# Optimization experiments

Measured on AMD Instinct MI355X. Metric: run time of the kernel, lower is better.

## Reference

```python
import jax, jax.numpy as jnp
import numpy as np

N_NODES = 20000
N_EDGES = 320000
N_RELS = 200
DESC_LEN = 16
DIM_G = 64
DIM_WORD = 300
DIM_HIDDEN = 256
H_DIR = DIM_HIDDEN // 2  # per-direction GRU hidden
N_CLASS = 2000
V_WORD = 30000
V_DESC = 30000
B, T = 4, 32


def setup_inputs() -> dict:
    key = jax.random.key(0)
    ks = jax.random.split(key, 24)
    inp = {}
    # index tensors (pad token is 0; generate tokens in [1, V) so all positions valid)
    inp['questions'] = jax.random.randint(ks[0], (B, T), 1, V_WORD)
    inp['node_descs'] = jax.random.randint(ks[1], (N_NODES, DESC_LEN), 1, V_DESC)
    inp['edge_src'] = jax.random.randint(ks[2], (N_EDGES,), 0, N_NODES)
    inp['edge_dst'] = jax.random.randint(ks[3], (N_EDGES,), 0, N_NODES)
    inp['edge_type'] = jax.random.randint(ks[4], (N_EDGES,), 0, N_RELS)
    # embeddings (normal with std 1/sqrt(dim) as in original init)
    inp['emb_word'] = jax.random.normal(ks[5], (V_WORD, DIM_WORD)) / np.sqrt(DIM_WORD)
    inp['emb_desc'] = jax.random.normal(ks[6], (V_DESC, DIM_G)) / np.sqrt(DIM_G)
    # BiGRU params (gates order r,z,n; concatenated along last dim)
    s = 0.1
    inp['Wx_f'] = jax.random.normal(ks[7], (DIM_WORD, 3 * H_DIR)) * s
    inp['Wh_f'] = jax.random.normal(ks[8], (H_DIR, 3 * H_DIR)) * s
    inp['bx_f'] = jnp.zeros((3 * H_DIR,))
    inp['bh_f'] = jnp.zeros((3 * H_DIR,))
    inp['Wx_b'] = jax.random.normal(ks[9], (DIM_WORD, 3 * H_DIR)) * s
    inp['Wh_b'] = jax.random.normal(ks[10], (H_DIR, 3 * H_DIR)) * s
    inp['bx_b'] = jnp.zeros((3 * H_DIR,))
    inp['bh_b'] = jnp.zeros((3 * H_DIR,))
    # lin_h_to_g (kaiming-ish scale)
    inp['W_hg'] = jax.random.normal(ks[11], (DIM_HIDDEN, DIM_G)) * np.sqrt(2.0 / DIM_HIDDEN)
    inp['b_hg'] = jnp.zeros((DIM_G,))
    # RGCN basis decomposition
    inp['bases'] = jax.random.normal(ks[12], (1, DIM_G, DIM_G)) * np.sqrt(1.0 / DIM_G)
    inp['w_comp'] = jax.random.normal(ks[13], (N_RELS, 1))
    inp['rgcn_bias'] = jnp.zeros((DIM_G,))
    # classifier
    inp['W1'] = jax.random.normal(ks[14], (DIM_G + DIM_HIDDEN, 1024)) * np.sqrt(2.0 / (DIM_G + DIM_HIDDEN))
    inp['b1'] = jnp.zeros((1024,))
    inp['W2'] = jax.random.normal(ks[15], (1024, N_CLASS)) * np.sqrt(2.0 / 1024)
    inp['b2'] = jnp.zeros((N_CLASS,))
    return inp


def _gru_last_hidden(x, mask, Wx, Wh, bx, bh):
    """Run a GRU over time; hidden only updates where mask is True.
    x: [B,T,D], mask: [B,T]. Returns final hidden [B,H]."""
    bsz = x.shape[0]
    h0 = jnp.zeros((bsz, Wh.shape[0]), x.dtype)
    gx_all = x @ Wx + bx  # [B,T,3H] precompute input gates

    def step(h, inputs):
        gx, mt = inputs  # [B,3H], [B]
        gh = h @ Wh + bh
        xr, xz, xn = jnp.split(gx, 3, axis=-1)
        hr, hz, hn = jnp.split(gh, 3, axis=-1)
        r = jax.nn.sigmoid(xr + hr)
        z = jax.nn.sigmoid(xz + hz)
        n = jnp.tanh(xn + r * hn)
        h_new = (1.0 - z) * n + z * h
        h = jnp.where(mt[:, None], h_new, h)
        return h, None

    hT, _ = jax.lax.scan(step, h0, (gx_all.transpose(1, 0, 2), mask.T))
    return hT


def _rel_graph_conv(h, edge_src, edge_dst, edge_type, bases, w_comp, bias):
    """Basis-decomposed RGCN layer (DGL RelGraphConv, norm=None, no self-loop).
    h: [B,N,G]. W_r = sum_k w_comp[r,k] * bases[k]."""
    n = h.shape[1]
    # project through each basis first: [B,N,K,O]
    hb = jnp.einsum('bng,kgo->bnko', h, bases)
    # per-edge message: gather src, combine with relation coefficients -> [B,E,O]
    msg = jnp.einsum('beko,ek->beo', hb[:, edge_src], w_comp[edge_type])
    # scatter-add to destination nodes
    agg = jax.vmap(lambda m: jax.ops.segment_sum(m, edge_dst, num_segments=n))(msg)
    return jax.nn.relu(agg + bias)


def reference(questions, node_descs, edge_src, edge_dst, edge_type,
              emb_word, emb_desc,
              Wx_f, Wh_f, bx_f, bh_f, Wx_b, Wh_b, bx_b, bh_b,
              W_hg, b_hg, bases, w_comp, rgcn_bias,
              W1, b1, W2, b2):
    # ---- question encoding (BiGRU over non-pad tokens; pad id = 0) ----
    mask = questions != 0  # [B,T]
    x = emb_word[questions]  # [B,T,Dw] (dropout is identity at eval)
    hf = _gru_last_hidden(x, mask, Wx_f, Wh_f, bx_f, bh_f)
    hb = _gru_last_hidden(x[:, ::-1], mask[:, ::-1], Wx_b, Wh_b, bx_b, bh_b)
    q_emb = jnp.concatenate([hf, hb], axis=-1)  # [B, dim_hidden]

    # ---- attention-weighted node features from descriptions ----
    desc_emb = emb_desc[node_descs]          # [N,L,G]
    q_g = q_emb @ W_hg + b_hg                # [B,G]
    attn1 = jax.nn.softmax(jnp.einsum('nlg,bg->bnl', desc_emb, q_g), axis=-1)
    node_feat = jnp.einsum('bnl,nlg->bng', attn1, desc_emb)  # [B,N,G]

    # ---- one RGCN hidden layer over the KB graph ----
    node_feat = _rel_graph_conv(node_feat, edge_src, edge_dst, edge_type,
                                bases, w_comp, rgcn_bias)

    # ---- attention pooling over nodes ----
    attn2 = jax.nn.softmax(jnp.einsum('bng,bg->bn', node_feat, q_g), axis=1)
    node_agg = jnp.einsum('bn,bng->bg', attn2, node_feat)    # [B,G]

    # ---- classifier ----
    feat = jnp.concatenate([node_agg, q_emb], axis=-1)       # [B, G+H]
    logits = jax.nn.relu(feat @ W1 + b1) @ W2 + b2           # [B, n_class]
    return logits
```

## Files before the change

### kernel.cpp

```cpp
#include <hip/hip_runtime.h>
#include <hip/hip_bf16.h>
#include <math.h>

typedef __hip_bfloat16 bf16;

#define NNODES 20000
#define NEDGES 320000
#define DLEN   16
#define G      64
#define DW     300
#define DH     256
#define HD     128
#define G3     384
#define NCLS   2000
#define NB     4
#define TT     32
#define A2BLK  1024
#define A2MID  64

#define NBLK_CVT  384
#define NBLK_GX2  1536
#define NBLK_HIST ((NEDGES + 255) / 256)
#define NBLK_SCAT ((NEDGES + 255) / 256)

__device__ __forceinline__ float ld(const float* p, size_t i) { return p[i]; }
__device__ __forceinline__ float ld(const bf16* p, size_t i) { return __bfloat162float(p[i]); }
__device__ __forceinline__ void st(float* p, size_t i, float v) { p[i] = v; }
__device__ __forceinline__ void st(bf16* p, size_t i, float v) { p[i] = __float2bfloat16(v); }
__device__ __forceinline__ float relu(float x) { return (x < 0.f) ? 0.f : x; }

struct __align__(8) bf4 { bf16 x, y, z, w; };

#define OFF_FLAG  ((size_t)0)
#define OFF_GX    (OFF_FLAG + 4)
#define OFF_WHF   (OFF_GX   + 2*NB*TT*G3)
#define OFF_QEMB  (OFF_WHF  + 2*HD*G3)
#define OFF_QG    (OFF_QEMB + NB*DH)
#define OFF_NF    (OFF_QG   + NB*G)
#define OFF_HB    (OFF_NF   + (size_t)NB*NNODES*G)
#define OFF_PART  (OFF_HB   + (size_t)NB*NNODES*G)
#define OFF_PART2 (OFF_PART + (size_t)A2BLK*NB*66)
#define OFF_DEG   (OFF_PART2+ (size_t)A2MID*NB*66)
#define OFF_OFFS  (OFF_DEG  + NNODES)
#define OFF_CUR   (OFF_OFFS + NNODES + 8)
#define OFF_SSRC  (OFF_CUR  + NNODES)
#define OFF_SCO   (OFF_SSRC + NEDGES)
#define OFF_HID   (OFF_SCO  + NEDGES)

__global__ void k_init(const unsigned* probe, int* flag, int* deg) {
    int i = blockIdx.x * 256 + threadIdx.x;
    if (i < NNODES) deg[i] = 0;
    if (blockIdx.x == 0 && threadIdx.x < 64) {
        int cnt = 0;
        for (int k = threadIdx.x; k < 4096; k += 64) {
            unsigned lo = probe[k] & 0xFFFFu;
            unsigned e = (lo >> 7) & 0xFFu;
            cnt += (e >= 0x66u && e <= 0x7Eu) ? 1 : 0;
        }
#pragma unroll
        for (int off = 1; off < 64; off <<= 1) cnt += __shfl_xor(cnt, off, 64);
        if (threadIdx.x == 0) *flag = (2 * cnt > 4096) ? 1 : 0;
    }
}

template <typename T>
__device__ void cvt_body(int id, const void* Whf_, const void* Whb_, float* whf) {
    if (id >= 2 * HD * G3) return;
    int d = id / (HD * G3), r = id % (HD * G3);
    const T* W = (const T*)(d ? Whb_ : Whf_);
    whf[id] = ld(W, (size_t)r);
}

template <typename T>
__device__ void gx2_body(int bx2, const int* questions, const void* emb_word_,
                         const void* Wxf_, const void* bxf_,
                         const void* Wxb_, const void* bxb_, float* gx,
                         float* xs, float* psum) {
    int tid = threadIdx.x;
    int jt = bx2 % 6;
    int rid = bx2 / 6;
    int step = rid & 31;
    int b = (rid >> 5) & 3;
    int d = rid >> 7;
    int t = d ? (TT - 1 - step) : step;
    int tok = questions[b * TT + t];
    const T* row = (const T*)emb_word_ + (size_t)tok * DW;
    for (int k = tid; k < DW; k += 256) xs[k] = ld(row, (size_t)k);
    __syncthreads();
    int lane = tid & 63, phase = tid >> 6;
    int j = jt * 64 + lane;
    const T* Wx = (const T*)(d ? Wxb_ : Wxf_);
    float acc = 0.f;
    int k0 = phase * 75;
#pragma unroll 15
    for (int kk = 0; kk < 75; kk++) {
        int k = k0 + kk;
        acc += xs[k] * ld(Wx, (size_t)k * G3 + j);
    }
    psum[tid] = acc;
    __syncthreads();
    if (phase == 0) {
        const T* bx = (const T*)(d ? bxb_ : bxf_);
        float tot = ld(bx, (size_t)j)
                  + psum[lane] + psum[64 + lane] + psum[128 + lane] + psum[192 + lane];
        gx[(size_t)rid * G3 + j] = tot;
    }
}

__global__ void k_prep(const int* flag, const void* Whf, const void* Whb, float* whf,
                       const int* questions, const void* emb_word,
                       const void* Wxf, const void* bxf,
                       const void* Wxb, const void* bxb, float* gx,
                       const int* edge_dst, int* deg) {
    __shared__ float xs[DW];
    __shared__ float psum[256];
    int bx = blockIdx.x;
    int tid = threadIdx.x;
    if (bx < NBLK_CVT) {
        int id = bx * 256 + tid;
        if (*flag) cvt_body<bf16>(id, Whf, Whb, whf);
        else       cvt_body<float>(id, Whf, Whb, whf);
    } else if (bx < NBLK_CVT + NBLK_GX2) {
        int bx2 = bx - NBLK_CVT;
        if (*flag) gx2_body<bf16>(bx2, questions, emb_word, Wxf, bxf, Wxb, bxb, gx, xs, psum);
        else       gx2_body<float>(bx2, questions, emb_word, Wxf, bxf, Wxb, bxb, gx, xs, psum);
    } else {
        int e = (bx - NBLK_CVT - NBLK_GX2) * 256 + tid;
        if (e < NEDGES) atomicAdd(&deg[edge_dst[e]], 1);
    }
}

template <typename T>
__device__ void gru_body(const int* questions, const float* gx, const float* whf,
                         const void* bhf_, const void* bhb_, float* qemb,
                         float* hsm, float* ghs) {
    int tid = threadIdx.x;
    int d = blockIdx.x >> 2, b = blockIdx.x & 3;
    int half = tid / G3, j = tid - half * G3;
    const float* wh = whf + (size_t)d * HD * G3 + (size_t)half * 64 * G3 + j;
    float w[64];
#pragma unroll
    for (int m = 0; m < 64; m++) w[m] = wh[(size_t)m * G3];
    const T* bh = (const T*)(d ? bhb_ : bhf_);
    float bhj = (half == 0) ? ld(bh, (size_t)j) : 0.f;
    if (tid < HD) hsm[tid] = 0.f;
    const float* gxb = gx + ((size_t)(d * NB + b)) * TT * G3;
    __syncthreads();
    const float4* h4 = (const float4*)(hsm + half * 64);
    for (int step = 0; step < TT; step++) {
        float acc = bhj;
#pragma unroll
        for (int m4 = 0; m4 < 16; m4++) {
            float4 hp = h4[m4];
            acc = fmaf(hp.x, w[4 * m4 + 0], acc);
            acc = fmaf(hp.y, w[4 * m4 + 1], acc);
            acc = fmaf(hp.z, w[4 * m4 + 2], acc);
            acc = fmaf(hp.w, w[4 * m4 + 3], acc);
        }
        ghs[half * G3 + j] = acc;
        __syncthreads();
        if (tid < HD) {
            const float* gxp = gxb + step * G3;
            int t = d ? (TT - 1 - step) : step;
            bool msk = questions[b * TT + t] != 0;
            float gr = ghs[tid] + ghs[G3 + tid];
            float gz = ghs[HD + tid] + ghs[G3 + HD + tid];
            float gn = ghs[2 * HD + tid] + ghs[G3 + 2 * HD + tid];
            float r = 1.f / (1.f + expf(-(gxp[tid] + gr)));
            float z = 1.f / (1.f + expf(-(gxp[HD + tid] + gz)));
            float n = tanhf(gxp[2 * HD + tid] + r * gn);
            float hn = (1.f - z) * n + z * hsm[tid];
            if (msk) hsm[tid] = hn;
        }
        __syncthreads();
    }
    if (tid < HD) qemb[b * DH + d * HD + tid] = hsm[tid];
}

__device__ void scan_body(const int* deg, int* offs, int* cur, int* wtot) {
    int t = threadIdx.x;
    int lane = t & 63, wave = t >> 6;
    int c[27];
    int base = t * 27;
    int run = 0;
#pragma unroll
    for (int i = 0; i < 27; i++) {
        int v = (base + i < NNODES) ? deg[base + i] : 0;
        c[i] = run;
        run += v;
    }
    int myrun = run, inc = run;
#pragma unroll
    for (int off = 1; off < 64; off <<= 1) {
        int u = __shfl_up(inc, off, 64);
        if (lane >= off) inc += u;
    }
    if (lane == 63) wtot[wave] = inc;
    __syncthreads();
    if (t == 0) {
        int s = 0;
#pragma unroll
        for (int i = 0; i < 12; i++) { int v = wtot[i]; wtot[i] = s; s += v; }
        offs[NNODES] = s;
    }
    __syncthreads();
    int ebase = wtot[wave] + inc - myrun;
#pragma unroll
    for (int i = 0; i < 27; i++) {
        if (base + i < NNODES) {
            offs[base + i] = ebase + c[i];
            cur[base + i] = ebase + c[i];
        }
    }
}

__global__ __launch_bounds__(2 * G3) void k_gru(const int* flag, const int* questions,
                                                const float* gx, const float* whf,
                                                const void* bhf, const void* bhb, float* qemb,
                                                const int* deg, int* offs, int* cur) {
    __shared__ __align__(16) float hsm[HD];
    __shared__ float ghs[2 * G3];
    __shared__ int wtot[12];
    if (blockIdx.x < 8) {
        if (*flag) gru_body<bf16>(questions, gx, whf, bhf, bhb, qemb, hsm, ghs);
        else       gru_body<float>(questions, gx, whf, bhf, bhb, qemb, hsm, ghs);
    } else {
        scan_body(deg, offs, cur, wtot);
    }
}

template <typename T>
__device__ void qg_body(const float* qemb, const void* W_hg_, const void* b_hg_, float* qg) {
    int tid = threadIdx.x;
    int b = tid >> 6, g = tid & 63;
    const T* W = (const T*)W_hg_;
    float acc = ld((const T*)b_hg_, (size_t)g);
#pragma unroll 4
    for (int i = 0; i < DH; i++) acc += qemb[b * DH + i] * ld(W, (size_t)i * G + g);
    qg[b * G + g] = acc;
}
__global__ void k_qg(const int* flag, const float* qemb, const void* W_hg,
                     const void* b_hg, float* qg) {
    if (*flag) qg_body<bf16>(qemb, W_hg, b_hg, qg);
    else       qg_body<float>(qemb, W_hg, b_hg, qg);
}

template <typename T>
__device__ void scatter_body(int e, const int* src, const int* dst, const int* typ,
                             const void* w_comp_, int* cur, int* ssrc, float* sco) {
    if (e < NEDGES) {
        int dd = dst[e];
        int pos = atomicAdd(&cur[dd], 1);
        ssrc[pos] = src[e];
        sco[pos] = ld((const T*)w_comp_, (size_t)typ[e]);
    }
}

template <typename T>
__device__ void attn1_body(int nb4, const int* node_descs, const void* emb_desc_,
                           const float* qg, bf16* nf16,
                           float* dsm, float* attn_s, float* qgs) {
    int tid = threadIdx.x;
    if (tid < NB * G) qgs[tid] = qg[tid];
    __syncthreads();
    const T* emb_desc = (const T*)emb_desc_;
    int w = tid >> 6, lane = tid & 63;
    int n = nb4 * 4 + w;
    float dreg[DLEN];
    const int* nd = node_descs + n * DLEN;
    float* dw = dsm + (size_t)w * DLEN * 68;
#pragma unroll
    for (int l = 0; l < DLEN; l++) {
        int idx = nd[l];
        float v = ld(emb_desc, (size_t)idx * G + lane);
        dreg[l] = v;
        dw[l * 68 + lane] = v;
    }
    int lb = lane >> 4, ll = lane & 15;
    float acc = 0.f;
#pragma unroll
    for (int i = 0; i < 16; i++) {
        float4 a = *(const float4*)&dw[ll * 68 + 4 * i];
        float4 q = *(const float4*)&qgs[lb * G + 4 * i];
        acc = fmaf(a.x, q.x, acc);
        acc = fmaf(a.y, q.y, acc);
        acc = fmaf(a.z, q.z, acc);
        acc = fmaf(a.w, q.w, acc);
    }
    float mx = acc;
#pragma unroll
    for (int off = 1; off < 16; off <<= 1) mx = fmaxf(mx, __shfl_xor(mx, off, 64));
    float e = expf(acc - mx);
    float s = e;
#pragma unroll
    for (int off = 1; off < 16; off <<= 1) s += __shfl_xor(s, off, 64);
    attn_s[w * 64 + lane] = e / s;
#pragma unroll
    for (int b = 0; b < NB; b++) {
        float a = 0.f;
#pragma unroll
        for (int l = 0; l < DLEN; l++) a += attn_s[w * 64 + b * 16 + l] * dreg[l];
        nf16[((size_t)b * NNODES + n) * G + lane] = __float2bfloat16(a);
    }
}

__global__ __launch_bounds__(256) void k_sc_attn1(const int* flag,
                                                  const int* src, const int* dst, const int* typ,
                                                  const void* w_comp, int* cur,
                                                  int* ssrc, float* sco,
                                                  const int* node_descs, const void* emb_desc,
                                                  const float* qg, bf16* nf16) {
    __shared__ __align__(16) float dsm[4 * DLEN * 68];
    __shared__ float attn_s[4 * 64];
    __shared__ __align__(16) float qgs[NB * G];
    int bx = blockIdx.x;
    if (bx < NBLK_SCAT) {
        int e = bx * 256 + threadIdx.x;
        if (*flag) scatter_body<bf16>(e, src, dst, typ, w_comp, cur, ssrc, sco);
        else       scatter_body<float>(e, src, dst, typ, w_comp, cur, ssrc, sco);
    } else {
        int nb4 = bx - NBLK_SCAT;
        if (*flag) attn1_body<bf16>(nb4, node_descs, emb_desc, qg, nf16, dsm, attn_s, qgs);
        else       attn1_body<float>(nb4, node_descs, emb_desc, qg, nf16, dsm, attn_s, qgs);
    }
}

template <typename T>
__device__ void hbg_body(const bf16* nf16, const void* bases_, bf16* hb16,
                         float* as, float* bs) {
    int tid = threadIdx.x;
    const T* bases = (const T*)bases_;
    for (int i = tid; i < G * G; i += 256) bs[(i >> 6) * 68 + (i & 63)] = ld(bases, (size_t)i);
    size_t r0 = (size_t)blockIdx.x * 64;
    const bf4* gA = (const bf4*)(nf16 + r0 * G);
#pragma unroll
    for (int i = 0; i < 4; i++) {
        int c = tid + i * 256;
        int row = c >> 4, col4 = c & 15;
        bf4 v = gA[c];
        float4 f;
        f.x = __bfloat162float(v.x);
        f.y = __bfloat162float(v.y);
        f.z = __bfloat162float(v.z);
        f.w = __bfloat162float(v.w);
        *(float4*)&as[row * 68 + col4 * 4] = f;
    }
    __syncthreads();
    int tx = tid & 15, ty = tid >> 4;
    float acc[4][4];
#pragma unroll
    for (int i = 0; i < 4; i++)
#pragma unroll
        for (int j = 0; j < 4; j++) acc[i][j] = 0.f;
#pragma unroll 4
    for (int g4 = 0; g4 < 16; g4++) {
        float4 b0 = *(const float4*)&bs[(4 * g4 + 0) * 68 + tx * 4];
        float4 b1 = *(const float4*)&bs[(4 * g4 + 1) * 68 + tx * 4];
        float4 b2 = *(const float4*)&bs[(4 * g4 + 2) * 68 + tx * 4];
        float4 b3 = *(const float4*)&bs[(4 * g4 + 3) * 68 + tx * 4];
#pragma unroll
        for (int i = 0; i < 4; i++) {
            float4 a = *(const float4*)&as[(ty * 4 + i) * 68 + g4 * 4];
            acc[i][0] = fmaf(a.x, b0.x, acc[i][0]);
            acc[i][0] = fmaf(a.y, b1.x, acc[i][0]);
            acc[i][0] = fmaf(a.z, b2.x, acc[i][0]);
            acc[i][0] = fmaf(a.w, b3.x, acc[i][0]);
            acc[i][1] = fmaf(a.x, b0.y, acc[i][1]);
            acc[i][1] = fmaf(a.y, b1.y, acc[i][1]);
            acc[i][1] = fmaf(a.z, b2.y, acc[i][1]);
            acc[i][1] = fmaf(a.w, b3.y, acc[i][1]);
            acc[i][2] = fmaf(a.x, b0.z, acc[i][2]);
            acc[i][2] = fmaf(a.y, b1.z, acc[i][2]);
            acc[i][2] = fmaf(a.z, b2.z, acc[i][2]);
            acc[i][2] = fmaf(a.w, b3.z, acc[i][2]);
            acc[i][3] = fmaf(a.x, b0.w, acc[i][3]);
            acc[i][3] = fmaf(a.y, b1.w, acc[i][3]);
            acc[i][3] = fmaf(a.z, b2.w, acc[i][3]);
            acc[i][3] = fmaf(a.w, b3.w, acc[i][3]);
        }
    }
#pragma unroll
    for (int i = 0; i < 4; i++) {
        size_t r = r0 + ty * 4 + i;
        int b = (int)(r / NNODES);
        int n = (int)(r - (size_t)b * NNODES);
        bf4 o;
        o.x = __float2bfloat16(acc[i][0]);
        o.y = __float2bfloat16(acc[i][1]);
        o.z = __float2bfloat16(acc[i][2]);
        o.w = __float2bfloat16(acc[i][3]);
        *(bf4*)&hb16[((size_t)n * NB + b) * G + tx * 4] = o;
    }
}
__global__ __launch_bounds__(256) void k_hbg(const int* flag, const bf16* nf16,
                                             const void* bases, bf16* hb16) {
    __shared__ __align__(16) float as[64 * 68];
    __shared__ __align__(16) float bs[64 * 68];
    if (*flag) hbg_body<bf16>(nf16, bases, hb16, as, bs);
    else       hbg_body<float>(nf16, bases, hb16, as, bs);
}

template <typename T>
__device__ void agg_body(const bf16* hb16, const int* offs, const int* ssrc,
                         const float* sco, const void* bias_, bf16* out_nf16) {
    int tid = threadIdx.x;
    int b = tid >> 6, g = tid & 63;
    int dn = blockIdx.x;
    int s0 = offs[dn], s1 = offs[dn + 1];
    int boff = b * G + g;
    float acc = 0.f;
    int p = s0;
    for (; p + 15 < s1; p += 16) {
        int ix[16]; float co[16]; float x[16];
#pragma unroll
        for (int k = 0; k < 16; k++) { ix[k] = ssrc[p + k]; co[k] = sco[p + k]; }
#pragma unroll
        for (int k = 0; k < 16; k++) x[k] = __bfloat162float(hb16[(size_t)ix[k] * (NB * G) + boff]);
#pragma unroll
        for (int k = 0; k < 16; k++) acc += co[k] * x[k];
    }
    for (; p + 7 < s1; p += 8) {
        int ix[8]; float co[8]; float x[8];
#pragma unroll
        for (int k = 0; k < 8; k++) { ix[k] = ssrc[p + k]; co[k] = sco[p + k]; }
#pragma unroll
        for (int k = 0; k < 8; k++) x[k] = __bfloat162float(hb16[(size_t)ix[k] * (NB * G) + boff]);
#pragma unroll
        for (int k = 0; k < 8; k++) acc += co[k] * x[k];
    }
    for (; p + 3 < s1; p += 4) {
        int ix[4]; float co[4]; float x[4];
#pragma unroll
        for (int k = 0; k < 4; k++) { ix[k] = ssrc[p + k]; co[k] = sco[p + k]; }
#pragma unroll
        for (int k = 0; k < 4; k++) x[k] = __bfloat162float(hb16[(size_t)ix[k] * (NB * G) + boff]);
#pragma unroll
        for (int k = 0; k < 4; k++) acc += co[k] * x[k];
    }
    for (; p < s1; p++)
        acc += sco[p] * __bfloat162float(hb16[(size_t)ssrc[p] * (NB * G) + boff]);
    out_nf16[((size_t)b * NNODES + dn) * G + g] =
        __float2bfloat16(relu(acc + ld((const T*)bias_, (size_t)g)));
}
__global__ __launch_bounds__(256) void k_agg(const int* flag, const bf16* hb16, const int* offs,
                                             const int* ssrc, const float* sco,
                                             const void* bias, bf16* out_nf16) {
    if (*flag) agg_body<bf16>(hb16, offs, ssrc, sco, bias, out_nf16);
    else       agg_body<float>(hb16, offs, ssrc, sco, bias, out_nf16);
}

__device__ __forceinline__ void a2_update(float& M, float& L, float& A, float p, float v) {
    if (p > M) {
        float s = expf(M - p);
        A *= s; L *= s; M = p;
    }
    float e = expf(p - M);
    L += e;
    A = fmaf(e, v, A);
}

__global__ __launch_bounds__(256) void k_attn2(const bf16* rg, const float* qg, float* part) {
    int tid = threadIdx.x;
    int b = tid >> 6, lane = tid & 63;
    float q = qg[b * G + lane];
    int chunk = (NNODES + A2BLK - 1) / A2BLK;
    int n0 = blockIdx.x * chunk;
    int n1 = min(n0 + chunk, NNODES);
    const bf16* base = rg + (size_t)b * NNODES * G + lane;
    float M = -3.4e38f, L = 0.f, A = 0.f;
    int n = n0;
    for (; n + 3 < n1; n += 4) {
        float v0 = __bfloat162float(base[(size_t)(n + 0) * G]);
        float v1 = __bfloat162float(base[(size_t)(n + 1) * G]);
        float v2 = __bfloat162float(base[(size_t)(n + 2) * G]);
        float v3 = __bfloat162float(base[(size_t)(n + 3) * G]);
        float p0 = v0 * q, p1 = v1 * q, p2 = v2 * q, p3 = v3 * q;
#pragma unroll
        for (int off = 32; off >= 1; off >>= 1) {
            p0 += __shfl_xor(p0, off, 64);
            p1 += __shfl_xor(p1, off, 64);
            p2 += __shfl_xor(p2, off, 64);
            p3 += __shfl_xor(p3, off, 64);
        }
        a2_update(M, L, A, p0, v0);
        a2_update(M, L, A, p1, v1);
        a2_update(M, L, A, p2, v2);
        a2_update(M, L, A, p3, v3);
    }
    for (; n < n1; n++) {
        float v = __bfloat162float(base[(size_t)n * G]);
        float p = v * q;
#pragma unroll
        for (int off = 32; off >= 1; off >>= 1) p += __shfl_xor(p, off, 64);
        a2_update(M, L, A, p, v);
    }
    float* pp = part + ((size_t)blockIdx.x * NB + b) * 66;
    if (lane == 0) { pp[0] = M; pp[1] = L; }
    pp[2 + lane] = A;
}

__global__ void k_attn2m(const float* part, float* part2) {
    int tid = threadIdx.x;
    int b = tid >> 6, lane = tid & 63;
    int grp = blockIdx.x;
    float M = -3.4e38f, L = 0.f, A = 0.f;
    for (int i = 0; i < A2BLK / A2MID; i++) {
        const float* pp = part + ((size_t)(grp * (A2BLK / A2MID) + i) * NB + b) * 66;
        float m = pp[0], l = pp[1], a = pp[2 + lane];
        float mn = fmaxf(M, m);
        float e1 = expf(M - mn), e2 = expf(m - mn);
        A = A * e1 + a * e2;
        L = L * e1 + l * e2;
        M = mn;
    }
    float* pq = part2 + ((size_t)grp * NB + b) * 66;
    if (lane == 0) { pq[0] = M; pq[1] = L; }
    pq[2 + lane] = A;
}

template <typename T>
__device__ void fc1_body(const float* part2, const float* qemb,
                         const void* W1_, const void* b1_, float* hid,
                         float* feat, float* psum) {
    int tid = threadIdx.x;
    int b = blockIdx.x >> 4, tile = blockIdx.x & 15;
    if (tid < 64) {
        float M = -3.4e38f, L = 0.f, A = 0.f;
        for (int p = 0; p < A2MID; p++) {
            const float* pp = part2 + ((size_t)p * NB + b) * 66;
            float m = pp[0], l = pp[1], a = pp[2 + tid];
            float mn = fmaxf(M, m);
            float e1 = expf(M - mn), e2 = expf(m - mn);
            A = A * e1 + a * e2;
            L = L * e1 + l * e2;
            M = mn;
        }
        feat[tid] = A / L;
        feat[tid + 256] = qemb[b * DH + tid + 192];
    } else {
        feat[tid] = qemb[b * DH + tid - G];
    }
    __syncthreads();
    int lane = tid & 63, phase = tid >> 6;
    int u = tile * 64 + lane;
    const T* W1 = (const T*)W1_;
    float acc = 0.f;
#pragma unroll 8
    for (int kk = 0; kk < 80; kk++) {
        int k = phase * 80 + kk;
        acc += feat[k] * ld(W1, (size_t)k * 1024 + u);
    }
    psum[tid] = acc;
    __syncthreads();
    if (phase == 0) {
        float tot = psum[lane] + psum[64 + lane] + psum[128 + lane] + psum[192 + lane]
                  + ld((const T*)b1_, (size_t)u);
        hid[b * 1024 + u] = relu(tot);
    }
}
__global__ __launch_bounds__(256) void k_fc1(const int* flag, const float* part2,
                                             const float* qemb, const void* W1, const void* b1,
                                             float* hid) {
    __shared__ float feat[320];
    __shared__ float psum[256];
    if (*flag) fc1_body<bf16>(part2, qemb, W1, b1, hid, feat, psum);
    else       fc1_body<float>(part2, qemb, W1, b1, hid, feat, psum);
}

template <typename T>
__device__ void fc2_body(const float* hid, const void* W2_, const void* b2_, void* out_,
                         float* hs, float* psum) {
    int tid = threadIdx.x;
    int tile = blockIdx.x;
#pragma unroll
    for (int i = 0; i < 16; i++) hs[tid + 256 * i] = hid[tid + 256 * i];
    __syncthreads();
    int lane = tid & 63, phase = tid >> 6;
    int c = tile * 64 + lane;
    bool ok = (c < NCLS);
    const T* W2 = (const T*)W2_;
    float a0 = 0.f, a1 = 0.f, a2 = 0.f, a3 = 0.f;
    if (ok) {
#pragma unroll 8
        for (int uu = 0; uu < 256; uu++) {
            int u = phase * 256 + uu;
            float w = ld(W2, (size_t)u * NCLS + c);
            a0 += hs[u] * w;
            a1 += hs[1024 + u] * w;
            a2 += hs[2048 + u] * w;
            a3 += hs[3072 + u] * w;
        }
    }
    psum[tid] = a0;
    psum[256 + tid] = a1;
    psum[512 + tid] = a2;
    psum[768 + tid] = a3;
    __syncthreads();
    if (phase == 0 && ok) {
        float bb = ld((const T*)b2_, (size_t)c);
#pragma unroll
        for (int b = 0; b < NB; b++) {
            float* ps = psum + b * 256;
            float tot = ps[lane] + ps[64 + lane] + ps[128 + lane] + ps[192 + lane] + bb;
            st((T*)out_, (size_t)b * NCLS + c, tot);
        }
    }
}
__global__ __launch_bounds__(256) void k_fc2(const int* flag, const float* hid,
                                             const void* W2, const void* b2v, void* out) {
    __shared__ float hs[4096];
    __shared__ float psum[1024];
    if (*flag) fc2_body<bf16>(hid, W2, b2v, out, hs, psum);
    else       fc2_body<float>(hid, W2, b2v, out, hs, psum);
}

extern "C" void kernel_launch(void* const* d_in, const int* in_sizes, int n_in,
                              void* d_out, int out_size, void* d_ws, size_t ws_size,
                              hipStream_t stream) {
    const int* questions  = (const int*)d_in[0];
    const int* node_descs = (const int*)d_in[1];
    const int* edge_src   = (const int*)d_in[2];
    const int* edge_dst   = (const int*)d_in[3];
    const int* edge_type  = (const int*)d_in[4];
    const void* emb_word  = d_in[5];
    const void* emb_desc  = d_in[6];
    const void* Wx_f = d_in[7];
    const void* Wh_f = d_in[8];
    const void* bx_f = d_in[9];
    const void* bh_f = d_in[10];
    const void* Wx_b = d_in[11];
    const void* Wh_b = d_in[12];
    const void* bx_b = d_in[13];
    const void* bh_b = d_in[14];
    const void* W_hg = d_in[15];
    const void* b_hg = d_in[16];
    const void* bases = d_in[17];
    const void* w_comp = d_in[18];
    const void* rgcn_bias = d_in[19];
    const void* W1 = d_in[20];
    const void* b1 = d_in[21];
    const void* W2 = d_in[22];
    const void* b2 = d_in[23];

    float* ws = (float*)d_ws;
    int*      flag  = (int*)(ws + OFF_FLAG);
    float*    gx    = ws + OFF_GX;
    float*    whf   = ws + OFF_WHF;
    float*    qemb  = ws + OFF_QEMB;
    float*    qg    = ws + OFF_QG;
    bf16*     nf16  = (bf16*)(ws + OFF_NF);
    bf16*     hb16  = (bf16*)(ws + OFF_HB);
    float*    part  = ws + OFF_PART;
    float*    part2 = ws + OFF_PART2;
    int*      deg   = (int*)(ws + OFF_DEG);
    int*      offs  = (int*)(ws + OFF_OFFS);
    int*      cur   = (int*)(ws + OFF_CUR);
    int*      ssrc  = (int*)(ws + OFF_SSRC);
    float*    sco   = ws + OFF_SCO;
    float*    hid   = ws + OFF_HID;

    hipLaunchKernelGGL(k_init, dim3(80), dim3(256), 0, stream,
                       (const unsigned*)emb_word, flag, deg);
    hipLaunchKernelGGL(k_prep, dim3(NBLK_CVT + NBLK_GX2 + NBLK_HIST), dim3(256), 0, stream,
                       flag, Wh_f, Wh_b, whf,
                       questions, emb_word, Wx_f, bx_f, Wx_b, bx_b, gx,
                       edge_dst, deg);
    hipLaunchKernelGGL(k_gru, dim3(9), dim3(2 * G3), 0, stream,
                       flag, questions, gx, whf, bh_f, bh_b, qemb, deg, offs, cur);
    hipLaunchKernelGGL(k_qg, dim3(1), dim3(256), 0, stream, flag, qemb, W_hg, b_hg, qg);
    hipLaunchKernelGGL(k_sc_attn1, dim3(NBLK_SCAT + NNODES / 4), dim3(256), 0, stream,
                       flag, edge_src, edge_dst, edge_type, w_comp, cur, ssrc, sco,
                       node_descs, emb_desc, qg, nf16);
    hipLaunchKernelGGL(k_hbg, dim3(NB * NNODES / 64), dim3(256), 0, stream,
                       flag, nf16, bases, hb16);
    hipLaunchKernelGGL(k_agg, dim3(NNODES), dim3(256), 0, stream,
                       flag, hb16, offs, ssrc, sco, rgcn_bias, nf16);
    hipLaunchKernelGGL(k_attn2, dim3(A2BLK), dim3(256), 0, stream, nf16, qg, part);
    hipLaunchKernelGGL(k_attn2m, dim3(A2MID), dim3(256), 0, stream, part, part2);
    hipLaunchKernelGGL(k_fc1, dim3(NB * 16), dim3(256), 0, stream,
                       flag, part2, qemb, W1, b1, hid);
    hipLaunchKernelGGL(k_fc2, dim3(32), dim3(256), 0, stream,
                       flag, hid, W2, b2, d_out);
}
```

Measured before the change: 323.1 us.

## Reuse histogram atomic ranks for CSR scatter and pack edge src/coef

The degree histogram now records each edge's atomicAdd return value as its rank, so the scatter pass computes its slot as offs[dst]+rank without a second round of atomics on a cursor array. Source index and relation coefficient are packed into one int2 array, so the aggregation kernel does one 8-byte load per edge instead of two separate loads. This adds an extra rank array write/read of NEDGES ints and changes the order of edges within a node's segment, which can alter float summation order.

```diff
diff --git a/kernel.cpp b/kernel.cpp
--- a/kernel.cpp
+++ b/kernel.cpp
@@ -42,10 +42,9 @@
 #define OFF_PART2 (OFF_PART + (size_t)A2BLK*NB*66)
 #define OFF_DEG   (OFF_PART2+ (size_t)A2MID*NB*66)
 #define OFF_OFFS  (OFF_DEG  + NNODES)
-#define OFF_CUR   (OFF_OFFS + NNODES + 8)
-#define OFF_SSRC  (OFF_CUR  + NNODES)
-#define OFF_SCO   (OFF_SSRC + NEDGES)
-#define OFF_HID   (OFF_SCO  + NEDGES)
+#define OFF_RANK  (OFF_OFFS + NNODES + 8)
+#define OFF_EPACK (OFF_RANK + NEDGES)
+#define OFF_HID   (OFF_EPACK + 2*(size_t)NEDGES)
 
 __global__ void k_init(const unsigned* probe, int* flag, int* deg) {
     int i = blockIdx.x * 256 + threadIdx.x;
@@ -111,7 +110,7 @@
                        const int* questions, const void* emb_word,
                        const void* Wxf, const void* bxf,
                        const void* Wxb, const void* bxb, float* gx,
-                       const int* edge_dst, int* deg) {
+                       const int* edge_dst, int* deg, int* rank) {
     __shared__ float xs[DW];
     __shared__ float psum[256];
     int bx = blockIdx.x;
@@ -126,7 +125,7 @@
         else       gx2_body<float>(bx2, questions, emb_word, Wxf, bxf, Wxb, bxb, gx, xs, psum);
     } else {
         int e = (bx - NBLK_CVT - NBLK_GX2) * 256 + tid;
-        if (e < NEDGES) atomicAdd(&deg[edge_dst[e]], 1);
+        if (e < NEDGES) rank[e] = atomicAdd(&deg[edge_dst[e]], 1);
     }
 }
 
@@ -177,7 +176,7 @@
     if (tid < HD) qemb[b * DH + d * HD + tid] = hsm[tid];
 }
 
-__device__ void scan_body(const int* deg, int* offs, int* cur, int* wtot) {
+__device__ void scan_body(const int* deg, int* offs, int* wtot) {
     int t = threadIdx.x;
     int lane = t & 63, wave = t >> 6;
     int c[27];
@@ -207,17 +206,14 @@
     int ebase = wtot[wave] + inc - myrun;
 #pragma unroll
     for (int i = 0; i < 27; i++) {
-        if (base + i < NNODES) {
-            offs[base + i] = ebase + c[i];
-            cur[base + i] = ebase + c[i];
-        }
+        if (base + i < NNODES) offs[base + i] = ebase + c[i];
     }
 }
 
 __global__ __launch_bounds__(2 * G3) void k_gru(const int* flag, const int* questions,
                                                 const float* gx, const float* whf,
                                                 const void* bhf, const void* bhb, float* qemb,
-                                                const int* deg, int* offs, int* cur) {
+                                                const int* deg, int* offs) {
     __shared__ __align__(16) float hsm[HD];
     __shared__ float ghs[2 * G3];
     __shared__ int wtot[12];
@@ -225,7 +221,7 @@
         if (*flag) gru_body<bf16>(questions, gx, whf, bhf, bhb, qemb, hsm, ghs);
         else       gru_body<float>(questions, gx, whf, bhf, bhb, qemb, hsm, ghs);
     } else {
-        scan_body(deg, offs, cur, wtot);
+        scan_body(deg, offs, wtot);
     }
 }
 
@@ -247,12 +243,14 @@
 
 template <typename T>
 __device__ void scatter_body(int e, const int* src, const int* dst, const int* typ,
-                             const void* w_comp_, int* cur, int* ssrc, float* sco) {
+                             const void* w_comp_, const int* offs, const int* rank,
+                             int2* epack) {
     if (e < NEDGES) {
-        int dd = dst[e];
-        int pos = atomicAdd(&cur[dd], 1);
-        ssrc[pos] = src[e];
-        sco[pos] = ld((const T*)w_comp_, (size_t)typ[e]);
+        int pos = offs[dst[e]] + rank[e];
+        int2 v;
+        v.x = src[e];
+        v.y = __float_as_int(ld((const T*)w_comp_, (size_t)typ[e]));
+        epack[pos] = v;
     }
 }
 
@@ -306,8 +304,8 @@
 
 __global__ __launch_bounds__(256) void k_sc_attn1(const int* flag,
                                                   const int* src, const int* dst, const int* typ,
-                                                  const void* w_comp, int* cur,
-                                                  int* ssrc, float* sco,
+                                                  const void* w_comp, const int* offs,
+                                                  const int* rank, int2* epack,
                                                   const int* node_descs, const void* emb_desc,
                                                   const float* qg, bf16* nf16) {
     __shared__ __align__(16) float dsm[4 * DLEN * 68];
@@ -316,8 +314,8 @@
     int bx = blockIdx.x;
     if (bx < NBLK_SCAT) {
         int e = bx * 256 + threadIdx.x;
-        if (*flag) scatter_body<bf16>(e, src, dst, typ, w_comp, cur, ssrc, sco);
-        else       scatter_body<float>(e, src, dst, typ, w_comp, cur, ssrc, sco);
+        if (*flag) scatter_body<bf16>(e, src, dst, typ, w_comp, offs, rank, epack);
+        else       scatter_body<float>(e, src, dst, typ, w_comp, offs, rank, epack);
     } else {
         int nb4 = bx - NBLK_SCAT;
         if (*flag) attn1_body<bf16>(nb4, node_descs, emb_desc, qg, nf16, dsm, attn_s, qgs);
@@ -401,8 +399,8 @@
 }
 
 template <typename T>
-__device__ void agg_body(const bf16* hb16, const int* offs, const int* ssrc,
-                         const float* sco, const void* bias_, bf16* out_nf16) {
+__device__ void agg_body(const bf16* hb16, const int* offs, const int2* epack,
+                         const void* bias_, bf16* out_nf16) {
     int tid = threadIdx.x;
     int b = tid >> 6, g = tid & 63;
     int dn = blockIdx.x;
@@ -411,42 +409,47 @@
     float acc = 0.f;
     int p = s0;
     for (; p + 15 < s1; p += 16) {
-        int ix[16]; float co[16]; float x[16];
-#pragma unroll
-        for (int k = 0; k < 16; k++) { ix[k] = ssrc[p + k]; co[k] = sco[p + k]; }
-#pragma unroll
-        for (int k = 0; k < 16; k++) x[k] = __bfloat162float(hb16[(size_t)ix[k] * (NB * G) + boff]);
-#pragma unroll
-        for (int k = 0; k < 16; k++) acc += co[k] * x[k];
+        int2 ev[16]; float x[16];
+#pragma unroll
+        for (int k = 0; k < 16; k++) ev[k] = epack[p + k];
+#pragma unroll
+        for (int k = 0; k < 16; k++)
+            x[k] = __bfloat162float(hb16[(size_t)ev[k].x * (NB * G) + boff]);
+#pragma unroll
+        for (int k = 0; k < 16; k++) acc += __int_as_float(ev[k].y) * x[k];
     }
     for (; p + 7 < s1; p += 8) {
-        int ix[8]; float co[8]; float x[8];
-#pragma unroll
-        for (int k = 0; k < 8; k++) { ix[k] = ssrc[p + k]; co[k] = sco[p + k]; }
-#pragma unroll
-        for (int k = 0; k < 8; k++) x[k] = __bfloat162float(hb16[(size_t)ix[k] * (NB * G) + boff]);
-#pragma unroll
-        for (int k = 0; k < 8; k++) acc += co[k] * x[k];
+        int2 ev[8]; float x[8];
+#pragma unroll
+        for (int k = 0; k < 8; k++) ev[k] = epack[p + k];
+#pragma unroll
+        for (int k = 0; k < 8; k++)
+            x[k] = __bfloat162float(hb16[(size_t)ev[k].x * (NB * G) + boff]);
+#pragma unroll
+        for (int k = 0; k < 8; k++) acc += __int_as_float(ev[k].y) * x[k];
     }
     for (; p + 3 < s1; p += 4) {
-        int ix[4]; float co[4]; float x[4];
-#pragma unroll
-        for (int k = 0; k < 4; k++) { ix[k] = ssrc[p + k]; co[k] = sco[p + k]; }
-#pragma unroll
-        for (int k = 0; k < 4; k++) x[k] = __bfloat162float(hb16[(size_t)ix[k] * (NB * G) + boff]);
-#pragma unroll
-        for (int k = 0; k < 4; k++) acc += co[k] * x[k];
-    }
-    for (; p < s1; p++)
-        acc += sco[p] * __bfloat162float(hb16[(size_t)ssrc[p] * (NB * G) + boff]);
+        int2 ev[4]; float x[4];
+#pragma unroll
+        for (int k = 0; k < 4; k++) ev[k] = epack[p + k];
+#pragma unroll
+        for (int k = 0; k < 4; k++)
+            x[k] = __bfloat162float(hb16[(size_t)ev[k].x * (NB * G) + boff]);
+#pragma unroll
+        for (int k = 0; k < 4; k++) acc += __int_as_float(ev[k].y) * x[k];
+    }
+    for (; p < s1; p++) {
+        int2 ev = epack[p];
+        acc += __int_as_float(ev.y) * __bfloat162float(hb16[(size_t)ev.x * (NB * G) + boff]);
+    }
     out_nf16[((size_t)b * NNODES + dn) * G + g] =
         __float2bfloat16(relu(acc + ld((const T*)bias_, (size_t)g)));
 }
 __global__ __launch_bounds__(256) void k_agg(const int* flag, const bf16* hb16, const int* offs,
-                                             const int* ssrc, const float* sco,
-                                             const void* bias, bf16* out_nf16) {
-    if (*flag) agg_body<bf16>(hb16, offs, ssrc, sco, bias, out_nf16);
-    else       agg_body<float>(hb16, offs, ssrc, sco, bias, out_nf16);
+                                             const int2* epack, const void* bias,
+                                             bf16* out_nf16) {
+    if (*flag) agg_body<bf16>(hb16, offs, epack, bias, out_nf16);
+    else       agg_body<float>(hb16, offs, epack, bias, out_nf16);
 }
 
 __device__ __forceinline__ void a2_update(float& M, float& L, float& A, float p, float v) {
@@ -654,9 +657,8 @@
     float*    part2 = ws + OFF_PART2;
     int*      deg   = (int*)(ws + OFF_DEG);
     int*      offs  = (int*)(ws + OFF_OFFS);
-    int*      cur   = (int*)(ws + OFF_CUR);
-    int*      ssrc  = (int*)(ws + OFF_SSRC);
-    float*    sco   = ws + OFF_SCO;
+    int*      rank  = (int*)(ws + OFF_RANK);
+    int2*     epack = (int2*)(ws + OFF_EPACK);
     float*    hid   = ws + OFF_HID;
 
     hipLaunchKernelGGL(k_init, dim3(80), dim3(256), 0, stream,
@@ -664,17 +666,17 @@
     hipLaunchKernelGGL(k_prep, dim3(NBLK_CVT + NBLK_GX2 + NBLK_HIST), dim3(256), 0, stream,
                        flag, Wh_f, Wh_b, whf,
                        questions, emb_word, Wx_f, bx_f, Wx_b, bx_b, gx,
-                       edge_dst, deg);
+                       edge_dst, deg, rank);
     hipLaunchKernelGGL(k_gru, dim3(9), dim3(2 * G3), 0, stream,
-                       flag, questions, gx, whf, bh_f, bh_b, qemb, deg, offs, cur);
+                       flag, questions, gx, whf, bh_f, bh_b, qemb, deg, offs);
     hipLaunchKernelGGL(k_qg, dim3(1), dim3(256), 0, stream, flag, qemb, W_hg, b_hg, qg);
     hipLaunchKernelGGL(k_sc_attn1, dim3(NBLK_SCAT + NNODES / 4), dim3(256), 0, stream,
-                       flag, edge_src, edge_dst, edge_type, w_comp, cur, ssrc, sco,
+                       flag, edge_src, edge_dst, edge_type, w_comp, offs, rank, epack,
                        node_descs, emb_desc, qg, nf16);
     hipLaunchKernelGGL(k_hbg, dim3(NB * NNODES / 64), dim3(256), 0, stream,
                        flag, nf16, bases, hb16);
     hipLaunchKernelGGL(k_agg, dim3(NNODES), dim3(256), 0, stream,
-                       flag, hb16, offs, ssrc, sco, rgcn_bias, nf16);
+                       flag, hb16, offs, epack, rgcn_bias, nf16);
     hipLaunchKernelGGL(k_attn2, dim3(A2BLK), dim3(256), 0, stream, nf16, qg, part);
     hipLaunchKernelGGL(k_attn2m, dim3(A2MID), dim3(256), 0, stream, part, part2);
     hipLaunchKernelGGL(k_fc1, dim3(NB * 16), dim3(256), 0, stream,
```

Measured after the change: 312.4 us. -3.3%, faster.
